# Optimization experiments

Measured on AMD Instinct MI355X. Metric: run time of the kernel, lower is better.

## Reference

```python
import jax, jax.numpy as jnp
import numpy as np
import math

EMBED = 1024
N_HEAD = 16
T_LEN = 2048
BATCH = 2
MLP_MULT = 4
EPS = 1e-5


def setup_inputs() -> dict:
    key = jax.random.key(0)
    ks = jax.random.split(key, 12)
    d = EMBED
    h = MLP_MULT * d
    s = 0.02
    return {
        "x": jax.random.normal(ks[0], (BATCH, T_LEN, d), dtype=jnp.float32),
        "ln1_scale": jnp.ones((d,), jnp.float32),
        "ln1_shift": jnp.zeros((d,), jnp.float32),
        "w_qkv": jax.random.normal(ks[1], (d, 3 * d), jnp.float32) * s,
        "b_qkv": jnp.zeros((3 * d,), jnp.float32),
        "ln2_scale": jnp.ones((d,), jnp.float32),
        "ln2_shift": jnp.zeros((d,), jnp.float32),
        "w_fc": jax.random.normal(ks[2], (d, h), jnp.float32) * s,
        "b_fc": jnp.zeros((h,), jnp.float32),
        "w_proj": jax.random.normal(ks[3], (h, d), jnp.float32) * s,
        "b_proj": jnp.zeros((d,), jnp.float32),
    }


def _layer_norm(x, scale, shift):
    mu = jnp.mean(x, axis=-1, keepdims=True)
    var = jnp.var(x, axis=-1, keepdims=True)
    return (x - mu) * jax.lax.rsqrt(var + EPS) * scale + shift


def _attention(h, w_qkv, b_qkv):
    B, T, C = h.shape
    hd = C // N_HEAD
    qkv = h @ w_qkv + b_qkv  # [B,T,3C]
    q, k, v = jnp.split(qkv, 3, axis=-1)
    q = q.reshape(B, T, N_HEAD, hd)
    k = k.reshape(B, T, N_HEAD, hd)
    v = v.reshape(B, T, N_HEAD, hd)
    scores = jnp.einsum("bthd,bshd->bhts", q, k) * (1.0 / math.sqrt(hd))
    causal = jnp.tril(jnp.ones((T, T), dtype=bool))
    scores = jnp.where(causal[None, None], scores, -jnp.inf)
    probs = jax.nn.softmax(scores, axis=-1)
    y = jnp.einsum("bhts,bshd->bthd", probs, v)
    return y.reshape(B, T, C)


def reference(x, ln1_scale, ln1_shift, w_qkv, b_qkv, ln2_scale, ln2_shift,
              w_fc, b_fc, w_proj, b_proj):
    x = x + _attention(_layer_norm(x, ln1_scale, ln1_shift), w_qkv, b_qkv)
    h = _layer_norm(x, ln2_scale, ln2_shift)
    # note: module names it 'gelu' but it's nn.ReLU()
    h = jax.nn.relu(h @ w_fc + b_fc) @ w_proj + b_proj
    return x + h
```

## Files before the change

### kernel.cpp

```cpp
#include <hip/hip_runtime.h>
#include <hip/hip_bf16.h>


typedef __bf16  bf16x8  __attribute__((ext_vector_type(8)));
typedef __bf16  bf16x4  __attribute__((ext_vector_type(4)));
typedef float   floatx4 __attribute__((ext_vector_type(4)));

#define T_LEN 2048
#define EMB   1024
#define NH    16
#define HD    64
#define HID   4096

#define GLOBAL_LOAD_LDS16(gp, lp) \
    __builtin_amdgcn_global_load_lds( \
        (const __attribute__((address_space(1))) void*)(gp), \
        (__attribute__((address_space(3))) void*)(lp), 16, 0, 0)

__global__ void transpose_cast(const float* __restrict__ in,
                               __bf16* __restrict__ out, int R, int C) {
    __shared__ float tile[32][33];
    int bc = blockIdx.x * 32;
    int br = blockIdx.y * 32;
    int tx = threadIdx.x;
    int ty = threadIdx.y;
    for (int i = 0; i < 32; i += 8) {
        tile[ty + i][tx] = in[(size_t)(br + ty + i) * C + bc + tx];
    }
    __syncthreads();
    for (int i = 0; i < 32; i += 8) {
        int c = bc + ty + i, r = br + tx;
        out[(size_t)c * R + r] = (__bf16)tile[tx][ty + i];
    }
}

__global__ __launch_bounds__(256)
void ln_kernel(const float* __restrict__ in, const float* __restrict__ sc,
               const float* __restrict__ sh, __bf16* __restrict__ out) {
    int row = blockIdx.x;
    const float* p = in + (size_t)row * EMB;
    int tid = threadIdx.x;
    int lane = tid & 63, wave = tid >> 6;
    float v[4];
    float s = 0.f, s2 = 0.f;
    for (int j = 0; j < 4; j++) {
        v[j] = p[tid + j * 256];
        s += v[j]; s2 += v[j] * v[j];
    }
    for (int m = 1; m < 64; m <<= 1) {
        s  += __shfl_xor(s, m);
        s2 += __shfl_xor(s2, m);
    }
    __shared__ float ssum[4], ssum2[4];
    if (lane == 0) { ssum[wave] = s; ssum2[wave] = s2; }
    __syncthreads();
    float tot  = ssum[0] + ssum[1] + ssum[2] + ssum[3];
    float tot2 = ssum2[0] + ssum2[1] + ssum2[2] + ssum2[3];
    float mean = tot * (1.f / EMB);
    float var  = tot2 * (1.f / EMB) - mean * mean;
    float rstd = rsqrtf(var + 1e-5f);
    for (int j = 0; j < 4; j++) {
        int c = tid + j * 256;
        out[(size_t)row * EMB + c] = (__bf16)((v[j] - mean) * rstd * sc[c] + sh[c]);
    }
}

__global__ __launch_bounds__(256)
void gemm_bt(const __bf16* __restrict__ A, const __bf16* __restrict__ Bt,
             const float* __restrict__ bias, const float* __restrict__ res,
             float* __restrict__ outF, __bf16* __restrict__ outB,
             int M, int N, int lda, int KL, int relu, int gx, int gz) {
    __shared__ __align__(16) __bf16 sA[2][128][32];
    __shared__ __align__(16) __bf16 sB[2][128][32];
    const int BUFE = 128 * 32;
    int tid  = threadIdx.x;
    int lane = tid & 63, wave = tid >> 6;
    int quad = lane >> 4, l16 = lane & 15;

    int i  = blockIdx.x;
    int c  = i & 7, m = i >> 3;
    int bx = m % gx;
    int p  = (m / gx) * 8 + c;
    int by = p / gz;
    int bz = p - by * gz;

    int bm = by * 128, bn = bx * 128;
    size_t k0 = (size_t)bz * KL;
    int wm = (wave & 1) * 64, wn = (wave >> 1) * 64;
    floatx4 acc[4][4] = {};

    int seg = wave * 2;
    int srow = seg * 16 + (lane >> 2);
    int scol = (lane & 3) * 8;
    const __bf16* gA0 = &A[(size_t)(bm + srow) * lda + k0 + scol];
    const __bf16* gB0 = &Bt[(size_t)(bn + srow) * lda + k0 + scol];
    __bf16* lA0 = &sA[0][seg * 16][0];
    __bf16* lB0 = &sB[0][seg * 16][0];

    GLOBAL_LOAD_LDS16(gA0, lA0);
    GLOBAL_LOAD_LDS16(gA0 + (size_t)16 * lda, lA0 + 16 * 32);
    GLOBAL_LOAD_LDS16(gB0, lB0);
    GLOBAL_LOAD_LDS16(gB0 + (size_t)16 * lda, lB0 + 16 * 32);

    int cur = 0;
    for (int kk = 0; kk < KL; kk += 32) {
        __syncthreads();
        if (kk + 32 < KL) {
            int no = (cur ^ 1) * BUFE;
            GLOBAL_LOAD_LDS16(gA0 + kk + 32, lA0 + no);
            GLOBAL_LOAD_LDS16(gA0 + kk + 32 + (size_t)16 * lda,
                              lA0 + no + 16 * 32);
            GLOBAL_LOAD_LDS16(gB0 + kk + 32, lB0 + no);
            GLOBAL_LOAD_LDS16(gB0 + kk + 32 + (size_t)16 * lda,
                              lB0 + no + 16 * 32);
        }
        bf16x8 af[4], bfr[4];
        for (int ii = 0; ii < 4; ii++)
            af[ii] = *(const bf16x8*)&sA[cur][wm + ii * 16 + l16][quad * 8];
        for (int j = 0; j < 4; j++)
            bfr[j] = *(const bf16x8*)&sB[cur][wn + j * 16 + l16][quad * 8];
        for (int ii = 0; ii < 4; ii++)
            for (int j = 0; j < 4; j++)
                acc[ii][j] = __builtin_amdgcn_mfma_f32_16x16x32_bf16(
                    af[ii], bfr[j], acc[ii][j], 0, 0, 0);
        cur ^= 1;
    }

    if (bias) {
        for (int ii = 0; ii < 4; ii++) {
            int row0 = bm + wm + ii * 16 + quad * 4;
            for (int j = 0; j < 4; j++) {
                int col = bn + wn + j * 16 + l16;
                float bv = bias[col];
                for (int r = 0; r < 4; r++) {
                    size_t idx = (size_t)(row0 + r) * N + col;
                    float cc = acc[ii][j][r] + bv;
                    if (relu) cc = fmaxf(cc, 0.f);
                    if (res)  cc += res[idx];
                    if (outF) outF[idx] = cc;
                    if (outB) outB[idx] = (__bf16)cc;
                }
            }
        }
    } else {
        __bf16* po = outB + (size_t)bz * M * N;
        for (int ii = 0; ii < 4; ii++) {
            int row0 = bm + wm + ii * 16 + quad * 4;
            for (int j = 0; j < 4; j++) {
                int col = bn + wn + j * 16 + l16;
                for (int r = 0; r < 4; r++)
                    po[(size_t)(row0 + r) * N + col] = (__bf16)acc[ii][j][r];
            }
        }
    }
}

__global__ __launch_bounds__(256)
void reduce_proj(const __bf16* __restrict__ pbuf, const float* __restrict__ x2,
                 const float* __restrict__ bias, float* __restrict__ out) {
    const size_t MN = (size_t)4096 * 1024;
    size_t i = (size_t)blockIdx.x * 256 + threadIdx.x;
    float4 r = ((const float4*)x2)[i];
    float4 bb = ((const float4*)bias)[i & 255];
    float acc0 = r.x + bb.x, acc1 = r.y + bb.y;
    float acc2 = r.z + bb.z, acc3 = r.w + bb.w;
    for (int k = 0; k < 4; k++) {
        bf16x4 pv = *(const bf16x4*)&pbuf[k * MN + i * 4];
        acc0 += (float)pv[0]; acc1 += (float)pv[1];
        acc2 += (float)pv[2]; acc3 += (float)pv[3];
    }
    float4 o = {acc0, acc1, acc2, acc3};
    ((float4*)out)[i] = o;
}

__global__ __launch_bounds__(256)
void gemm_bt_n64(const __bf16* __restrict__ A, const __bf16* __restrict__ Bt,
                 const float* __restrict__ bias, const float* __restrict__ res,
                 float* __restrict__ outF, __bf16* __restrict__ outB,
                 int M, int N, int K, int relu) {
    __shared__ __align__(16) __bf16 sA[128][40];
    __shared__ __align__(16) __bf16 sB[64][40];
    int tid  = threadIdx.x;
    int lane = tid & 63, wave = tid >> 6;
    int quad = lane >> 4, l16 = lane & 15;
    int bm = blockIdx.y * 128, bn = blockIdx.x * 64;
    int wm = (wave & 1) * 64, wn = (wave >> 1) * 32;
    floatx4 acc[4][2] = {};

    int srow = tid >> 2;
    int scol = (tid & 3) * 8;
    const __bf16* gA = &A[(size_t)(bm + srow) * K + scol];
    const __bf16* gB = &Bt[(size_t)(bn + srow) * K + scol];

    uint4 ra0 = *(const uint4*)gA;
    uint4 ra1 = *(const uint4*)(gA + (size_t)64 * K);
    uint4 rb0 = *(const uint4*)gB;

    for (int kk = 0; kk < K; kk += 32) {
        __syncthreads();
        *(uint4*)&sA[srow][scol]      = ra0;
        *(uint4*)&sA[srow + 64][scol] = ra1;
        *(uint4*)&sB[srow][scol]      = rb0;
        __syncthreads();
        {
            int kn = (kk + 32 < K) ? kk + 32 : kk;
            ra0 = *(const uint4*)(gA + kn);
            ra1 = *(const uint4*)(gA + kn + (size_t)64 * K);
            rb0 = *(const uint4*)(gB + kn);
        }
        bf16x8 af[4], bfr[2];
        for (int i = 0; i < 4; i++)
            af[i] = *(const bf16x8*)&sA[wm + i * 16 + l16][quad * 8];
        for (int j = 0; j < 2; j++)
            bfr[j] = *(const bf16x8*)&sB[wn + j * 16 + l16][quad * 8];
        for (int i = 0; i < 4; i++)
            for (int j = 0; j < 2; j++)
                acc[i][j] = __builtin_amdgcn_mfma_f32_16x16x32_bf16(
                    af[i], bfr[j], acc[i][j], 0, 0, 0);
    }

    for (int i = 0; i < 4; i++) {
        int row0 = bm + wm + i * 16 + quad * 4;
        for (int j = 0; j < 2; j++) {
            int col = bn + wn + j * 16 + l16;
            float bv = bias[col];
            for (int r = 0; r < 4; r++) {
                size_t idx = (size_t)(row0 + r) * N + col;
                float c = acc[i][j][r] + bv;
                if (relu) c = fmaxf(c, 0.f);
                if (res)  c += res[idx];
                if (outF) outF[idx] = c;
                if (outB) outB[idx] = (__bf16)c;
            }
        }
    }
}

__global__ __launch_bounds__(256)
void attn_kernel(const __bf16* __restrict__ qkv, const float* __restrict__ x,
                 float* __restrict__ x2) {
    __shared__ __align__(16) __bf16 sK[2][64][72];
    __shared__ __align__(16) __bf16 sVt[2][64][72];
    __shared__ __align__(16) __bf16 sP[4][16][72];
    const int tid  = threadIdx.x;
    const int lane = tid & 63, wave = tid >> 6;
    const int quad = lane >> 4, l16 = lane & 15;

    int i = blockIdx.x;
    int c = i & 7, m = i >> 3;
    const int bh = (m & 3) * 8 + c;
    const int qb = 31 - (m >> 2);
    const int h  = bh & (NH - 1);
    const int b  = bh >> 4;
    const size_t rowbase = (size_t)b * T_LEN;
    const int qrow = qb * 64 + wave * 16;

    const float kQScale = 0.125f * 1.44269504088896f;
    bf16x8 ones;
    for (int j = 0; j < 8; j++) ones[j] = (__bf16)1.0f;

    const int key0 = tid >> 3, m8 = tid & 7;
    const int key1 = key0 + 32;
    const __bf16* kp0 = qkv + (rowbase + key0) * 3072 + h * HD + m8 * 8 + 1024;
    const __bf16* kp1 = qkv + (rowbase + key1) * 3072 + h * HD + m8 * 8 + 1024;
    const int pc0 = ((key0 >> 3) ^ m8) * 8 + (key0 & 7);
    const int pc1 = ((key1 >> 3) ^ m8) * 8 + (key1 & 7);

    bf16x8 qf[2];
    for (int ks = 0; ks < 2; ks++) {
        bf16x8 raw = *(const bf16x8*)&qkv[(rowbase + qrow + l16) * 3072
                                          + h * HD + ks * 32 + quad * 8];
        for (int j = 0; j < 8; j++)
            qf[ks][j] = (__bf16)((float)raw[j] * kQScale);
    }

    floatx4 o[4] = {}, ol = {};

    const int ntiles = qb + 1;
    const size_t TSTEP = (size_t)64 * 3072;

    uint4 kr0 = *(const uint4*)kp0;
    uint4 kr1 = *(const uint4*)kp1;
    uint4 vr0 = *(const uint4*)(kp0 + 1024);
    uint4 vr1 = *(const uint4*)(kp1 + 1024);
    {
        *(uint4*)&sK[0][key0][m8 * 8] = kr0;
        *(uint4*)&sK[0][key1][m8 * 8] = kr1;
        bf16x8 v0 = *(bf16x8*)&vr0, v1 = *(bf16x8*)&vr1;
        for (int j = 0; j < 8; j++) sVt[0][m8 * 8 + j][pc0] = v0[j];
        for (int j = 0; j < 8; j++) sVt[0][m8 * 8 + j][pc1] = v1[j];
    }
    {
        size_t o1 = (ntiles > 1) ? TSTEP : 0;
        kr0 = *(const uint4*)(kp0 + o1);
        kr1 = *(const uint4*)(kp1 + o1);
        vr0 = *(const uint4*)(kp0 + o1 + 1024);
        vr1 = *(const uint4*)(kp1 + o1 + 1024);
    }
    __syncthreads();

    for (int kt = 0; kt < ntiles; kt++) {
        const int cur = kt & 1, nxt = cur ^ 1;
        if (kt + 1 < ntiles) {
            *(uint4*)&sK[nxt][key0][m8 * 8] = kr0;
            *(uint4*)&sK[nxt][key1][m8 * 8] = kr1;
            bf16x8 v0 = *(bf16x8*)&vr0, v1 = *(bf16x8*)&vr1;
            for (int j = 0; j < 8; j++) sVt[nxt][m8 * 8 + j][pc0] = v0[j];
            for (int j = 0; j < 8; j++) sVt[nxt][m8 * 8 + j][pc1] = v1[j];
            size_t offn = (size_t)((kt + 2 < ntiles) ? kt + 2 : kt + 1) * TSTEP;
            kr0 = *(const uint4*)(kp0 + offn);
            kr1 = *(const uint4*)(kp1 + offn);
            vr0 = *(const uint4*)(kp0 + offn + 1024);
            vr1 = *(const uint4*)(kp1 + offn + 1024);
        }

        floatx4 s_acc[4] = {};
        for (int jt = 0; jt < 4; jt++)
            for (int ks = 0; ks < 2; ks++) {
                bf16x8 kf = *(const bf16x8*)&sK[cur][jt * 16 + l16]
                                              [ks * 32 + quad * 8];
                s_acc[jt] = __builtin_amdgcn_mfma_f32_16x16x32_bf16(
                    qf[ks], kf, s_acc[jt], 0, 0, 0);
            }

        if (kt == qb) {
            const int tq0 = qrow + quad * 4;
            const int k0 = kt * 64;
            for (int jt = 0; jt < 4; jt++) {
                int key = k0 + jt * 16 + l16;
                for (int r = 0; r < 4; r++) {
                    float sv = (key <= tq0 + r) ? s_acc[jt][r] : -1e30f;
                    float pv = __builtin_amdgcn_exp2f(fminf(sv, 30.f));
                    sP[wave][quad * 4 + r][jt * 16 + l16] = (__bf16)pv;
                }
            }
        } else {
            for (int jt = 0; jt < 4; jt++)
                for (int r = 0; r < 4; r++) {
                    float pv = __builtin_amdgcn_exp2f(fminf(s_acc[jt][r], 30.f));
                    sP[wave][quad * 4 + r][jt * 16 + l16] = (__bf16)pv;
                }
        }

        for (int kp = 0; kp < 2; kp++) {
            bf16x8 pf = *(const bf16x8*)&sP[wave][l16][kp * 32 + quad * 8];
            ol = __builtin_amdgcn_mfma_f32_16x16x32_bf16(pf, ones, ol, 0, 0, 0);
            for (int jt2 = 0; jt2 < 4; jt2++) {
                int d = jt2 * 16 + l16;
                int pg = (kp * 4 + quad) ^ (d >> 3);
                bf16x8 vf = *(const bf16x8*)&sVt[cur][d][pg * 8];
                o[jt2] = __builtin_amdgcn_mfma_f32_16x16x32_bf16(
                    pf, vf, o[jt2], 0, 0, 0);
            }
        }
        __syncthreads();
    }

    float inv[4];
    for (int r = 0; r < 4; r++) inv[r] = __builtin_amdgcn_rcpf(ol[r]);
    for (int jt2 = 0; jt2 < 4; jt2++) {
        for (int r = 0; r < 4; r++) {
            int tq  = qrow + quad * 4 + r;
            int col = h * HD + jt2 * 16 + l16;
            size_t gi = (rowbase + tq) * EMB + col;
            x2[gi] = x[gi] + o[jt2][r] * inv[r];
        }
    }
}

extern "C" void kernel_launch(void* const* d_in, const int* in_sizes, int n_in,
                              void* d_out, int out_size, void* d_ws, size_t ws_size,
                              hipStream_t stream) {
    const float* x      = (const float*)d_in[0];
    const float* ln1_s  = (const float*)d_in[1];
    const float* ln1_b  = (const float*)d_in[2];
    const float* w_qkv  = (const float*)d_in[3];
    const float* b_qkv  = (const float*)d_in[4];
    const float* ln2_s  = (const float*)d_in[5];
    const float* ln2_b  = (const float*)d_in[6];
    const float* w_fc   = (const float*)d_in[7];
    const float* b_fc   = (const float*)d_in[8];
    const float* w_proj = (const float*)d_in[9];
    const float* b_proj = (const float*)d_in[10];
    float* out = (float*)d_out;

    const int M = 2 * T_LEN;
    char* ws = (char*)d_ws;
    size_t off = 0;
    auto alloc = [&](size_t bytes) {
        void* p = ws + off; off += (bytes + 255) & ~(size_t)255; return p;
    };
    __bf16* wpj_t  = (__bf16*)alloc((size_t)1024 * 4096 * 2);
    float*  x2     = (float*) alloc((size_t)M * 1024 * 4);
    __bf16* hfc    = (__bf16*)alloc((size_t)M * 4096 * 2);
    size_t mark = off;
    __bf16* wqkv_t = (__bf16*)alloc((size_t)3072 * 1024 * 2);
    __bf16* wfc_t  = (__bf16*)alloc((size_t)4096 * 1024 * 2);
    __bf16* h1     = (__bf16*)alloc((size_t)M * 1024 * 2);
    __bf16* h2     = (__bf16*)alloc((size_t)M * 1024 * 2);
    __bf16* qkvb   = (__bf16*)alloc((size_t)M * 3072 * 2);
    __bf16* pbuf = (__bf16*)(ws + mark);
    size_t need = mark + (size_t)4 * M * 1024 * 2;
    bool can_split = ws_size >= need;

    dim3 tb(32, 8);
    transpose_cast<<<dim3(3072 / 32, 1024 / 32), tb, 0, stream>>>(w_qkv, wqkv_t, 1024, 3072);
    transpose_cast<<<dim3(4096 / 32, 1024 / 32), tb, 0, stream>>>(w_fc,  wfc_t,  1024, 4096);
    transpose_cast<<<dim3(1024 / 32, 4096 / 32), tb, 0, stream>>>(w_proj, wpj_t, 4096, 1024);

    ln_kernel<<<M, 256, 0, stream>>>(x, ln1_s, ln1_b, h1);

    gemm_bt<<<24 * 32, 256, 0, stream>>>(
        h1, wqkv_t, b_qkv, nullptr, nullptr, qkvb, M, 3072, 1024, 1024, 0,
        24, 1);

    attn_kernel<<<1024, 256, 0, stream>>>(qkvb, x, x2);

    ln_kernel<<<M, 256, 0, stream>>>(x2, ln2_s, ln2_b, h2);

    gemm_bt<<<32 * 32, 256, 0, stream>>>(
        h2, wfc_t, b_fc, nullptr, nullptr, hfc, M, 4096, 1024, 1024, 1,
        32, 1);

    if (can_split) {
        gemm_bt<<<8 * 32 * 4, 256, 0, stream>>>(
            hfc, wpj_t, nullptr, nullptr, nullptr, pbuf, M, 1024, 4096, 1024, 0,
            8, 4);
        reduce_proj<<<(M * 1024 / 4) / 256, 256, 0, stream>>>(
            pbuf, x2, b_proj, out);
    } else {
        gemm_bt_n64<<<dim3(1024 / 64, M / 128), 256, 0, stream>>>(
            hfc, wpj_t, b_proj, x2, out, nullptr, M, 1024, 4096, 0);
    }
}
```

Before: 327.8 us.

## Replace 128x128 GEMM with 256x256 tile, 512-thread kernel using swizzled LDS

The 128x128x32 bf16 GEMM becomes a 256x256x64 tile run by 512 threads (8 waves, each computing 128x64). LDS staging uses an XOR-swizzled layout to avoid bank conflicts, with explicit vmcnt waits, barriers, and setprio around MFMA blocks to overlap loads and compute. All three GEMM launches switch to the new kernel with adjusted grids. Larger tiles raise arithmetic intensity and cut global traffic. The trade-off is 128 KB of LDS and high register pressure (128 accumulator floats), and only 192 to 256 blocks, which limits occupancy and wave fill across CUs.

```diff
diff --git a/kernel.cpp b/kernel.cpp
--- a/kernel.cpp
+++ b/kernel.cpp
@@ -65,14 +65,14 @@
     }
 }
 
-__global__ __launch_bounds__(256)
-void gemm_bt(const __bf16* __restrict__ A, const __bf16* __restrict__ Bt,
+__global__ __launch_bounds__(512)
+void gemm256(const __bf16* __restrict__ A, const __bf16* __restrict__ Bt,
              const float* __restrict__ bias, const float* __restrict__ res,
              float* __restrict__ outF, __bf16* __restrict__ outB,
              int M, int N, int lda, int KL, int relu, int gx, int gz) {
-    __shared__ __align__(16) __bf16 sA[2][128][32];
-    __shared__ __align__(16) __bf16 sB[2][128][32];
-    const int BUFE = 128 * 32;
+    __shared__ __align__(16) __bf16 sA[2][256][64];
+    __shared__ __align__(16) __bf16 sB[2][256][64];
+    const int BUFE = 256 * 64;
     int tid  = threadIdx.x;
     int lane = tid & 63, wave = tid >> 6;
     int quad = lane >> 4, l16 = lane & 15;
@@ -84,57 +84,140 @@
     int by = p / gz;
     int bz = p - by * gz;
 
-    int bm = by * 128, bn = bx * 128;
+    int bm = by * 256, bn = bx * 256;
     size_t k0 = (size_t)bz * KL;
-    int wm = (wave & 1) * 64, wn = (wave >> 1) * 64;
-    floatx4 acc[4][4] = {};
-
-    int seg = wave * 2;
-    int srow = seg * 16 + (lane >> 2);
-    int scol = (lane & 3) * 8;
-    const __bf16* gA0 = &A[(size_t)(bm + srow) * lda + k0 + scol];
-    const __bf16* gB0 = &Bt[(size_t)(bn + srow) * lda + k0 + scol];
-    __bf16* lA0 = &sA[0][seg * 16][0];
-    __bf16* lB0 = &sB[0][seg * 16][0];
-
-    GLOBAL_LOAD_LDS16(gA0, lA0);
-    GLOBAL_LOAD_LDS16(gA0 + (size_t)16 * lda, lA0 + 16 * 32);
-    GLOBAL_LOAD_LDS16(gB0, lB0);
-    GLOBAL_LOAD_LDS16(gB0 + (size_t)16 * lda, lB0 + 16 * 32);
-
-    int cur = 0;
-    for (int kk = 0; kk < KL; kk += 32) {
-        __syncthreads();
-        if (kk + 32 < KL) {
-            int no = (cur ^ 1) * BUFE;
-            GLOBAL_LOAD_LDS16(gA0 + kk + 32, lA0 + no);
-            GLOBAL_LOAD_LDS16(gA0 + kk + 32 + (size_t)16 * lda,
-                              lA0 + no + 16 * 32);
-            GLOBAL_LOAD_LDS16(gB0 + kk + 32, lB0 + no);
-            GLOBAL_LOAD_LDS16(gB0 + kk + 32 + (size_t)16 * lda,
-                              lB0 + no + 16 * 32);
-        }
-        bf16x8 af[4], bfr[4];
-        for (int ii = 0; ii < 4; ii++)
-            af[ii] = *(const bf16x8*)&sA[cur][wm + ii * 16 + l16][quad * 8];
-        for (int j = 0; j < 4; j++)
-            bfr[j] = *(const bf16x8*)&sB[cur][wn + j * 16 + l16][quad * 8];
-        for (int ii = 0; ii < 4; ii++)
-            for (int j = 0; j < 4; j++)
-                acc[ii][j] = __builtin_amdgcn_mfma_f32_16x16x32_bf16(
-                    af[ii], bfr[j], acc[ii][j], 0, 0, 0);
-        cur ^= 1;
-    }
+    int wm = (wave >> 2) * 128, wn = (wave & 3) * 64;
+
+    floatx4 acc[8][4] = {};
+
+    int srow  = tid >> 3;
+    int sslot = (tid & 7) ^ (srow & 7);
+    const __bf16* gA = A  + (size_t)(bm + srow) * lda + k0 + sslot * 8;
+    const __bf16* gB = Bt + (size_t)(bn + srow) * lda + k0 + sslot * 8;
+    __bf16* lA = &sA[0][0][0] + wave * 512;
+    __bf16* lB = &sB[0][0][0] + wave * 512;
+    const size_t rstep = (size_t)64 * lda;
+
+#define STAGE256(nb, ko) do { \
+    GLOBAL_LOAD_LDS16(gA + (ko),             lA + (nb) * BUFE); \
+    GLOBAL_LOAD_LDS16(gB + (ko),             lB + (nb) * BUFE); \
+    GLOBAL_LOAD_LDS16(gA + (ko) + rstep,     lA + (nb) * BUFE + 4096); \
+    GLOBAL_LOAD_LDS16(gB + (ko) + rstep,     lB + (nb) * BUFE + 4096); \
+    GLOBAL_LOAD_LDS16(gA + (ko) + 2 * rstep, lA + (nb) * BUFE + 8192); \
+    GLOBAL_LOAD_LDS16(gB + (ko) + 2 * rstep, lB + (nb) * BUFE + 8192); \
+    GLOBAL_LOAD_LDS16(gA + (ko) + 3 * rstep, lA + (nb) * BUFE + 12288); \
+    GLOBAL_LOAD_LDS16(gB + (ko) + 3 * rstep, lB + (nb) * BUFE + 12288); \
+} while (0)
+
+    STAGE256(0, (size_t)0);
+
+    int xs0  = ((quad) ^ (l16 & 7)) * 8;
+    int xs1  = ((4 + quad) ^ (l16 & 7)) * 8;
+    int aoff = (wm + l16) * 64;
+    int boff = (wn + l16) * 64;
+
+    const int nt = KL / 64;
+    for (int t = 0; t < nt; ++t) {
+        const int cur = t & 1;
+        __builtin_amdgcn_s_barrier();
+        asm volatile("" ::: "memory");
+        if (t + 1 < nt) {
+            STAGE256(cur ^ 1, (size_t)(t + 1) * 64);
+            asm volatile("s_waitcnt vmcnt(8)" ::: "memory");
+        } else {
+            asm volatile("s_waitcnt vmcnt(0)" ::: "memory");
+        }
+        __builtin_amdgcn_s_barrier();
+        asm volatile("" ::: "memory");
+        __builtin_amdgcn_sched_barrier(0);
+
+        const __bf16* sAc = &sA[0][0][0] + cur * BUFE;
+        const __bf16* sBc = &sB[0][0][0] + cur * BUFE;
+
+        bf16x8 a0[4][2], a1[4][2], b0[2][2], b1[2][2];
+
+        #pragma unroll
+        for (int mi = 0; mi < 4; ++mi) {
+            a0[mi][0] = *(const bf16x8*)(sAc + aoff + mi * 1024 + xs0);
+            a0[mi][1] = *(const bf16x8*)(sAc + aoff + mi * 1024 + xs1);
+        }
+        #pragma unroll
+        for (int nj = 0; nj < 2; ++nj) {
+            b0[nj][0] = *(const bf16x8*)(sBc + boff + nj * 1024 + xs0);
+            b0[nj][1] = *(const bf16x8*)(sBc + boff + nj * 1024 + xs1);
+        }
+        __builtin_amdgcn_s_setprio(1);
+        #pragma unroll
+        for (int mi = 0; mi < 4; ++mi)
+            #pragma unroll
+            for (int nj = 0; nj < 2; ++nj) {
+                acc[mi][nj] = __builtin_amdgcn_mfma_f32_16x16x32_bf16(
+                    a0[mi][0], b0[nj][0], acc[mi][nj], 0, 0, 0);
+                acc[mi][nj] = __builtin_amdgcn_mfma_f32_16x16x32_bf16(
+                    a0[mi][1], b0[nj][1], acc[mi][nj], 0, 0, 0);
+            }
+        __builtin_amdgcn_s_setprio(0);
+
+        #pragma unroll
+        for (int nj = 0; nj < 2; ++nj) {
+            b1[nj][0] = *(const bf16x8*)(sBc + boff + (2 + nj) * 1024 + xs0);
+            b1[nj][1] = *(const bf16x8*)(sBc + boff + (2 + nj) * 1024 + xs1);
+        }
+        __builtin_amdgcn_s_setprio(1);
+        #pragma unroll
+        for (int mi = 0; mi < 4; ++mi)
+            #pragma unroll
+            for (int nj = 0; nj < 2; ++nj) {
+                acc[mi][2 + nj] = __builtin_amdgcn_mfma_f32_16x16x32_bf16(
+                    a0[mi][0], b1[nj][0], acc[mi][2 + nj], 0, 0, 0);
+                acc[mi][2 + nj] = __builtin_amdgcn_mfma_f32_16x16x32_bf16(
+                    a0[mi][1], b1[nj][1], acc[mi][2 + nj], 0, 0, 0);
+            }
+        __builtin_amdgcn_s_setprio(0);
+
+        #pragma unroll
+        for (int mi = 0; mi < 4; ++mi) {
+            a1[mi][0] = *(const bf16x8*)(sAc + aoff + (4 + mi) * 1024 + xs0);
+            a1[mi][1] = *(const bf16x8*)(sAc + aoff + (4 + mi) * 1024 + xs1);
+        }
+        __builtin_amdgcn_s_setprio(1);
+        #pragma unroll
+        for (int mi = 0; mi < 4; ++mi)
+            #pragma unroll
+            for (int nj = 0; nj < 2; ++nj) {
+                acc[4 + mi][2 + nj] = __builtin_amdgcn_mfma_f32_16x16x32_bf16(
+                    a1[mi][0], b1[nj][0], acc[4 + mi][2 + nj], 0, 0, 0);
+                acc[4 + mi][2 + nj] = __builtin_amdgcn_mfma_f32_16x16x32_bf16(
+                    a1[mi][1], b1[nj][1], acc[4 + mi][2 + nj], 0, 0, 0);
+            }
+        __builtin_amdgcn_s_setprio(0);
+
+        __builtin_amdgcn_s_setprio(1);
+        #pragma unroll
+        for (int mi = 0; mi < 4; ++mi)
+            #pragma unroll
+            for (int nj = 0; nj < 2; ++nj) {
+                acc[4 + mi][nj] = __builtin_amdgcn_mfma_f32_16x16x32_bf16(
+                    a1[mi][0], b0[nj][0], acc[4 + mi][nj], 0, 0, 0);
+                acc[4 + mi][nj] = __builtin_amdgcn_mfma_f32_16x16x32_bf16(
+                    a1[mi][1], b0[nj][1], acc[4 + mi][nj], 0, 0, 0);
+            }
+        __builtin_amdgcn_s_setprio(0);
+    }
+#undef STAGE256
 
     if (bias) {
-        for (int ii = 0; ii < 4; ii++) {
-            int row0 = bm + wm + ii * 16 + quad * 4;
-            for (int j = 0; j < 4; j++) {
-                int col = bn + wn + j * 16 + l16;
+        #pragma unroll
+        for (int mi = 0; mi < 8; ++mi) {
+            int row0 = bm + wm + mi * 16 + quad * 4;
+            #pragma unroll
+            for (int nj = 0; nj < 4; ++nj) {
+                int col = bn + wn + nj * 16 + l16;
                 float bv = bias[col];
-                for (int r = 0; r < 4; r++) {
+                #pragma unroll
+                for (int r = 0; r < 4; ++r) {
                     size_t idx = (size_t)(row0 + r) * N + col;
-                    float cc = acc[ii][j][r] + bv;
+                    float cc = acc[mi][nj][r] + bv;
                     if (relu) cc = fmaxf(cc, 0.f);
                     if (res)  cc += res[idx];
                     if (outF) outF[idx] = cc;
@@ -144,12 +227,15 @@
         }
     } else {
         __bf16* po = outB + (size_t)bz * M * N;
-        for (int ii = 0; ii < 4; ii++) {
-            int row0 = bm + wm + ii * 16 + quad * 4;
-            for (int j = 0; j < 4; j++) {
-                int col = bn + wn + j * 16 + l16;
-                for (int r = 0; r < 4; r++)
-                    po[(size_t)(row0 + r) * N + col] = (__bf16)acc[ii][j][r];
+        #pragma unroll
+        for (int mi = 0; mi < 8; ++mi) {
+            int row0 = bm + wm + mi * 16 + quad * 4;
+            #pragma unroll
+            for (int nj = 0; nj < 4; ++nj) {
+                int col = bn + wn + nj * 16 + l16;
+                #pragma unroll
+                for (int r = 0; r < 4; ++r)
+                    po[(size_t)(row0 + r) * N + col] = (__bf16)acc[mi][nj][r];
             }
         }
     }
@@ -410,22 +496,22 @@
 
     ln_kernel<<<M, 256, 0, stream>>>(x, ln1_s, ln1_b, h1);
 
-    gemm_bt<<<24 * 32, 256, 0, stream>>>(
+    gemm256<<<192, 512, 0, stream>>>(
         h1, wqkv_t, b_qkv, nullptr, nullptr, qkvb, M, 3072, 1024, 1024, 0,
-        24, 1);
+        12, 1);
 
     attn_kernel<<<1024, 256, 0, stream>>>(qkvb, x, x2);
 
     ln_kernel<<<M, 256, 0, stream>>>(x2, ln2_s, ln2_b, h2);
 
-    gemm_bt<<<32 * 32, 256, 0, stream>>>(
+    gemm256<<<256, 512, 0, stream>>>(
         h2, wfc_t, b_fc, nullptr, nullptr, hfc, M, 4096, 1024, 1024, 1,
-        32, 1);
+        16, 1);
 
     if (can_split) {
-        gemm_bt<<<8 * 32 * 4, 256, 0, stream>>>(
+        gemm256<<<256, 512, 0, stream>>>(
             hfc, wpj_t, nullptr, nullptr, nullptr, pbuf, M, 1024, 4096, 1024, 0,
-            8, 4);
+            4, 4);
         reduce_proj<<<(M * 1024 / 4) / 256, 256, 0, stream>>>(
             pbuf, x2, b_proj, out);
     } else {
```

Measured after the change: 303.7 us. -7.3%, faster.
